# Kernel tuning notes

Hardware: AMD Instinct MI355X
Metric: run time of the kernel (lower is better)

Reference implementation:

```python
import jax, jax.numpy as jnp
import numpy as np

BN_EPS = 1e-5


def setup_inputs() -> dict:
    key = jax.random.key(0)
    ks = jax.random.split(key, 8)
    B, N, D = 16, 16384, 64
    NP, NS = 1024, 32
    inp = {
        "xyz": jax.random.normal(ks[0], (B, 3, N), dtype=jnp.float32),
        "points": jax.random.normal(ks[1], (B, D, N), dtype=jnp.float32),
        "fps_init": jax.random.randint(ks[2], (B,), 0, N, dtype=jnp.int32),
        "group_idx": jax.random.randint(ks[3], (B, NP, NS), 0, N, dtype=jnp.int32),
    }
    chans = [67, 64, 128, 128]
    for i in range(3):
        cin, cout = chans[i], chans[i + 1]
        wk = jax.random.fold_in(ks[4], i)
        inp[f"W{i}"] = jax.random.normal(wk, (cout, cin), dtype=jnp.float32) * (1.0 / np.sqrt(cin))
        inp[f"b{i}"] = jnp.zeros((cout,), dtype=jnp.float32)
        inp[f"g{i}"] = jnp.ones((cout,), dtype=jnp.float32)
        inp[f"be{i}"] = jnp.zeros((cout,), dtype=jnp.float32)
    return inp


def _fps(x, init_far, npoint):
    # x: [B,N,3]; iterative furthest point sampling, npoint sequential steps
    B, N, _ = x.shape

    def step(carry, _):
        dist, far = carry
        c = jnp.take_along_axis(x, far[:, None, None], axis=1)  # [B,1,3]
        d = jnp.sum((x - c) ** 2, axis=-1)                       # [B,N]
        dist = jnp.minimum(dist, d)
        return (dist, jnp.argmax(dist, axis=-1).astype(far.dtype)), far

    init = (jnp.full((B, N), 1e10, dtype=x.dtype), init_far)
    _, cents = jax.lax.scan(step, init, None, length=npoint)
    return cents.T  # [B, npoint]


def _conv_bn_relu(h, W, b, g, be):
    # h: [B, np, ns, Cin]; 1x1 conv == channel matmul; BN (training stats) over (B,np,ns)
    y = jnp.einsum('bskc,oc->bsko', h, W) + b
    m = y.mean(axis=(0, 1, 2))
    v = y.var(axis=(0, 1, 2))
    y = (y - m) * jax.lax.rsqrt(v + BN_EPS) * g + be
    return jax.nn.relu(y)


def reference(xyz, points, fps_init, group_idx,
              W0, b0, g0, be0, W1, b1, g1, be1, W2, b2, g2, be2):
    x = jnp.transpose(xyz, (0, 2, 1))     # [B,N,3]
    p = jnp.transpose(points, (0, 2, 1))  # [B,N,D]
    B, N, _ = x.shape
    NP, NS = group_idx.shape[1], group_idx.shape[2]

    cents = _fps(x, fps_init, NP)                                   # [B,NP]
    new_xyz = jnp.take_along_axis(x, cents[:, :, None], axis=1)     # [B,NP,3]

    flat = group_idx.reshape(B, NP * NS)
    gx = jnp.take_along_axis(x, flat[:, :, None], axis=1).reshape(B, NP, NS, 3)
    gp = jnp.take_along_axis(p, flat[:, :, None], axis=1).reshape(B, NP, NS, -1)
    h = jnp.concatenate([gx, gp], axis=-1)  # [B,NP,NS,67]

    h = _conv_bn_relu(h, W0, b0, g0, be0)
    h = _conv_bn_relu(h, W1, b1, g1, be1)
    h = _conv_bn_relu(h, W2, b2, g2, be2)
    new_points = h.max(axis=2)              # max over nsample -> [B,NP,Cout]

    return jnp.transpose(new_xyz, (0, 2, 1)), jnp.transpose(new_points, (0, 2, 1))
```

## Files before the change

kernel.cpp:

```cpp
#include <hip/hip_runtime.h>

typedef short bf16x8 __attribute__((ext_vector_type(8)));
typedef float f32x4 __attribute__((ext_vector_type(4)));
typedef float f32x2 __attribute__((ext_vector_type(2)));
typedef unsigned short u16;
typedef unsigned int u32;
typedef unsigned long long u64;

#define NPTS 16384
#define NPOINT 1024
#define STOT 524288
#define NCB 240
#define NW  960

__device__ __forceinline__ u16 f2bf(float f){
  u32 u = __builtin_bit_cast(u32, f);
  u += 0x7fffu + ((u >> 16) & 1u);
  return (u16)(u >> 16);
}
__device__ __forceinline__ float bf2f(u16 u){
  u32 x = ((u32)u) << 16;
  return __builtin_bit_cast(float, x);
}

template<int CTRL>
__device__ __forceinline__ float dpp_maxf(float v){
  int x = __builtin_amdgcn_update_dpp(0, __builtin_bit_cast(int, v), CTRL, 0xf, 0xf, true);
  return fmaxf(v, __builtin_bit_cast(float, x));
}
template<int CTRL>
__device__ __forceinline__ u64 dpp_max(u64 key){
  u32 lo = (u32)key, hi = (u32)(key >> 32);
  u32 lo1 = (u32)__builtin_amdgcn_update_dpp(0, (int)lo, CTRL, 0xf, 0xf, true);
  u32 hi1 = (u32)__builtin_amdgcn_update_dpp(0, (int)hi, CTRL, 0xf, 0xf, true);
  u64 k1 = ((u64)hi1 << 32) | (u64)lo1;
  return (k1 > key) ? k1 : key;
}
__device__ __forceinline__ u64 packkey(float d, int idx){
  return ((u64)__builtin_bit_cast(u32, d) << 32) | (u64)(u32)(~(u32)idx);
}

__device__ __forceinline__ void arrive(u32* c){
  __hip_atomic_fetch_add(c, 1u, __ATOMIC_RELEASE, __HIP_MEMORY_SCOPE_AGENT);
}
__device__ __forceinline__ void waitc(u32* c, u32 tgt){
  while (__hip_atomic_load(c, __ATOMIC_ACQUIRE, __HIP_MEMORY_SCOPE_AGENT) < tgt)
    __builtin_amdgcn_s_sleep(16);
}

struct FpsS  { uint2 wkey[2][16]; };
struct ConvS { float lsum[128]; float lsqr[128]; float av[128]; float dv[128]; };
union SMemU  { FpsS fps; ConvS conv; };

__device__ __forceinline__ bf16x8 load_bn_relu(const u16* __restrict__ row, int ko,
                                               const float* __restrict__ av,
                                               const float* __restrict__ dv){
  uint4 r = *(const uint4*)(row + ko);
  u32 w[4] = {r.x, r.y, r.z, r.w};
  bf16x8 out;
#pragma unroll
  for (int jj = 0; jj < 8; jj++){
    u16 us = (u16)(w[jj >> 1] >> ((jj & 1) * 16));
    float h = fmaxf(fmaf(av[ko + jj], bf2f(us), dv[ko + jj]), 0.f);
    out[jj] = (short)f2bf(h);
  }
  return out;
}

__global__ void zero_kernel(u32* __restrict__ ctrs){
  if (threadIdx.x < 64) ctrs[threadIdx.x] = 0;
}

__global__ __launch_bounds__(1024, 4) void mega_kernel(
    const float* __restrict__ xyz, const float* __restrict__ points,
    const int* __restrict__ finit, const int* __restrict__ gidx,
    const float* __restrict__ W0, const float* __restrict__ g0v, const float* __restrict__ be0,
    const float* __restrict__ W1, const float* __restrict__ g1v, const float* __restrict__ be1,
    const float* __restrict__ W2, const float* __restrict__ g2v, const float* __restrict__ be2,
    float* __restrict__ out0, float* __restrict__ out1,
    u16* __restrict__ XP, u16* __restrict__ y0, u16* __restrict__ y1,
    float* __restrict__ maxb, float* __restrict__ minb,
    float* __restrict__ statsF,
    u16* __restrict__ W0bf, u16* __restrict__ W1bf, u16* __restrict__ W2bf,
    u32* __restrict__ ctrs){
  __shared__ SMemU sm;
  const int t = threadIdx.x;
  const int wave = t >> 6, lane = t & 63;

  if (blockIdx.x < 16){
    const int b = blockIdx.x;
    const float* xb = xyz + (size_t)b * 3 * NPTS;
    f32x2 px[8], py[8], pz[8], dist[8];
#pragma unroll
    for (int j = 0; j < 8; j++){
      f32x2 x, y, z;
#pragma unroll
      for (int h = 0; h < 2; h++){
        int n = ((2*j + h) << 10) + t;
        x[h] = xb[n];
        y[h] = xb[NPTS + n];
        z[h] = xb[2*NPTS + n];
      }
      px[j] = x; py[j] = y; pz[j] = z;
      f32x2 big = {1e10f, 1e10f};
      dist[j] = big;
    }
    int nb = finit[b];
    float ccx = xb[nb], ccy = xb[NPTS + nb], ccz = xb[2*NPTS + nb];
    for (int it = 0; it < NPOINT; it++){
      const int p = it & 1;
      if (t == 0){
        out0[((size_t)b*3 + 0)*NPOINT + it] = ccx;
        out0[((size_t)b*3 + 1)*NPOINT + it] = ccy;
        out0[((size_t)b*3 + 2)*NPOINT + it] = ccz;
      }
      float bv = -1.f; int bk = 0;
      {
#pragma clang fp contract(off)
        f32x2 cx2 = {ccx, ccx}, cy2 = {ccy, ccy}, cz2 = {ccz, ccz};
#pragma unroll
        for (int j = 0; j < 8; j++){
          f32x2 dx = px[j] - cx2;
          f32x2 dy = py[j] - cy2;
          f32x2 dz = pz[j] - cz2;
          f32x2 dd = dx*dx + dy*dy + dz*dz;
          f32x2 dm = __builtin_elementwise_min(dist[j], dd);
          dist[j] = dm;
          bool g0 = dm.x > bv;
          bv = g0 ? dm.x : bv;  bk = g0 ? (2*j)   : bk;
          bool g1 = dm.y > bv;
          bv = g1 ? dm.y : bv;  bk = g1 ? (2*j+1) : bk;
        }
      }
      float m = bv;
      m = dpp_maxf<0xB1>(m);
      m = dpp_maxf<0x4E>(m);
      m = dpp_maxf<0x141>(m);
      m = dpp_maxf<0x140>(m);
      m = dpp_maxf<0x142>(m);
      m = dpp_maxf<0x143>(m);
      float ms = __builtin_bit_cast(float, __builtin_amdgcn_readlane(__builtin_bit_cast(int, m), 63));
      u64 mk = __ballot(bv == ms);
      u32 widx;
      if (__popcll(mk) == 1){
        int L = (int)__builtin_ctzll(mk);
        int kwin = __builtin_amdgcn_readlane(bk, L);
        widx = (u32)((kwin << 10) + (wave << 6) + L);
      } else {
        u64 key = packkey(bv, (bk << 10) + t);
        key = dpp_max<0xB1>(key); key = dpp_max<0x4E>(key);
        key = dpp_max<0x141>(key); key = dpp_max<0x140>(key);
        key = dpp_max<0x142>(key); key = dpp_max<0x143>(key);
        u32 lo = (u32)__builtin_amdgcn_readlane((int)(u32)key, 63);
        widx = ~lo;
      }
      if (lane == 0){
        uint2 wk; wk.x = widx; wk.y = __builtin_bit_cast(u32, ms);
        sm.fps.wkey[p][wave] = wk;
      }
      __syncthreads();
      uint2 wk = sm.fps.wkey[p][lane & 15];
      float wv = __builtin_bit_cast(float, wk.y);
      float g4 = wv;
      g4 = dpp_maxf<0xB1>(g4); g4 = dpp_maxf<0x4E>(g4);
      g4 = dpp_maxf<0x141>(g4); g4 = dpp_maxf<0x140>(g4);
      float gms = __builtin_bit_cast(float, __builtin_amdgcn_readfirstlane(__builtin_bit_cast(int, g4)));
      u64 mk2 = __ballot(wv == gms);
      u32 lo16 = (u32)mk2 & 0xFFFFu;
      if (__popc(lo16) == 1){
        int w = (int)__builtin_ctz(lo16);
        nb = __builtin_amdgcn_readlane((int)wk.x, w);
      } else {
        u64 k2 = ((u64)wk.y << 32) | (u64)(u32)(~wk.x);
        k2 = dpp_max<0xB1>(k2); k2 = dpp_max<0x4E>(k2);
        k2 = dpp_max<0x141>(k2); k2 = dpp_max<0x140>(k2);
        u32 lo = (u32)__builtin_amdgcn_readfirstlane((int)(u32)k2);
        nb = (int)~lo;
      }
      nb = __builtin_amdgcn_readfirstlane(nb);
      ccx = xb[nb]; ccy = xb[NPTS + nb]; ccz = xb[2*NPTS + nb];
    }
    return;
  }

  const int cb = blockIdx.x - 16;
  const int lw = wave & 3, g = wave >> 2;
  const int Wk = cb*4 + g;
  const int lrow = lane & 15, lq = lane >> 4;
  float* bsum0 = statsF;          float* bsqr0 = statsF + 8192;
  float* bsum1 = statsF + 16384;  float* bsqr1 = statsF + 24576;
  float* bsum2 = statsF + 32768;  float* bsqr2 = statsF + 40960;
  float* a0 = statsF + 49152;       float* d0 = a0 + 128;
  float* a1 = statsF + 49152 + 256; float* d1 = a1 + 128;
  float* a2 = statsF + 49152 + 512; float* d2 = a2 + 128;

  for (u32 idx = (u32)cb*1024u + t; idx < 16u*16384u; idx += (u32)NCB*1024u){
    u32 b = idx >> 14, n = idx & 16383u;
    const float* xb = xyz + (size_t)b*3*NPTS + n;
    const float* pb = points + (size_t)b*64*NPTS + n;
    u16* dst = XP + ((size_t)b*NPTS + n)*96;
#pragma unroll
    for (int half = 0; half < 2; half++){
      u32 w[24];
#pragma unroll
      for (int q = 0; q < 24; q++){
        int c0 = half*48 + 2*q, c1 = c0 + 1;
        float f0 = (c0 < 3) ? xb[(size_t)c0*NPTS] : (c0 < 67) ? pb[(size_t)(c0-3)*NPTS] : 0.f;
        float f1 = (c1 < 3) ? xb[(size_t)c1*NPTS] : (c1 < 67) ? pb[(size_t)(c1-3)*NPTS] : 0.f;
        w[q] = (u32)f2bf(f0) | ((u32)f2bf(f1) << 16);
      }
#pragma unroll
      for (int q = 0; q < 6; q++){
        uint4 v; v.x = w[4*q]; v.y = w[4*q+1]; v.z = w[4*q+2]; v.w = w[4*q+3];
        *(uint4*)(dst + half*48 + q*8) = v;
      }
    }
  }
  if (cb == 0){
    for (int i = t; i < 64*96; i += 1024){
      int nn = i / 96, kk = i % 96;
      W0bf[i] = (kk < 67) ? f2bf(W0[nn*67 + kk]) : (u16)0;
    }
    for (int i = t; i < 128*64; i += 1024) W1bf[i] = f2bf(W1[i]);
    for (int i = t; i < 128*128; i += 1024) W2bf[i] = f2bf(W2[i]);
  }
  if (cb == 1){
    for (int i = t; i < 49152; i += 1024) statsF[i] = 0.f;
  }
  __threadfence();
  __syncthreads();
  if (t == 0){ arrive(&ctrs[0]); waitc(&ctrs[0], NCB); }
  __syncthreads();

  if (t < 128){ sm.conv.lsum[t] = 0.f; sm.conv.lsqr[t] = 0.f; }
  __syncthreads();
  for (int j2 = Wk; j2 < 4096; j2 += NW){
    const int b = j2 >> 8;
    const size_t srow = (size_t)j2 * 128;
    const int gbase = b*32768 + (j2 & 255)*128;
    const int m0 = lw*32 + lrow, m1 = m0 + 16;
    const int p0 = gidx[gbase + m0];
    const int p1 = gidx[gbase + m1];
    const bf16x8* ar0 = (const bf16x8*)(XP + ((size_t)b*NPTS + p0)*96);
    const bf16x8* ar1 = (const bf16x8*)(XP + ((size_t)b*NPTS + p1)*96);
    f32x4 acc[2][4];
#pragma unroll
    for (int mt = 0; mt < 2; mt++)
#pragma unroll
      for (int nt = 0; nt < 4; nt++){ f32x4 z = {0.f,0.f,0.f,0.f}; acc[mt][nt] = z; }
#pragma unroll
    for (int ks = 0; ks < 3; ks++){
      bf16x8 af0 = ar0[ks*4 + lq];
      bf16x8 af1 = ar1[ks*4 + lq];
#pragma unroll
      for (int nt = 0; nt < 4; nt++){
        bf16x8 bb = *(const bf16x8*)(W0bf + (nt*16 + lrow)*96 + ks*32 + lq*8);
        acc[0][nt] = __builtin_amdgcn_mfma_f32_16x16x32_bf16(af0, bb, acc[0][nt], 0, 0, 0);
        acc[1][nt] = __builtin_amdgcn_mfma_f32_16x16x32_bf16(af1, bb, acc[1][nt], 0, 0, 0);
      }
    }
#pragma unroll
    for (int nt = 0; nt < 4; nt++){
      float s = 0.f, s2 = 0.f;
#pragma unroll
      for (int mt = 0; mt < 2; mt++){
#pragma unroll
        for (int i = 0; i < 4; i++){
          float u = acc[mt][nt][i];
          s += u; s2 = fmaf(u, u, s2);
          int m = lw*32 + mt*16 + lq*4 + i;
          y0[(srow + m)*64 + nt*16 + lrow] = f2bf(u);
        }
      }
      s  += __shfl_xor(s, 16, 64);  s  += __shfl_xor(s, 32, 64);
      s2 += __shfl_xor(s2, 16, 64); s2 += __shfl_xor(s2, 32, 64);
      if (lane < 16){ atomicAdd(&sm.conv.lsum[nt*16 + lane], s); atomicAdd(&sm.conv.lsqr[nt*16 + lane], s2); }
    }
  }
  __syncthreads();
  if (t < 64){
    atomicAdd(&bsum0[(cb & 63)*128 + t], sm.conv.lsum[t]);
    atomicAdd(&bsqr0[(cb & 63)*128 + t], sm.conv.lsqr[t]);
  }
  __threadfence();
  __syncthreads();
  if (t == 0) arrive(&ctrs[1]);
  if (cb == 0){
    if (t == 0) waitc(&ctrs[1], NCB);
    __syncthreads();
    if (t < 64){
      float s = 0.f, s2 = 0.f;
      for (int k = 0; k < 64; k++){ s += bsum0[k*128 + t]; s2 += bsqr0[k*128 + t]; }
      const float inv = 1.f / (float)STOT;
      float m = s * inv, v = s2 * inv - m*m;
      float aa = g0v[t] / sqrtf(v + 1e-5f);
      a0[t] = aa; d0[t] = be0[t] - m*aa;
    }
    __threadfence();
    __syncthreads();
    if (t == 0) arrive(&ctrs[2]);
  }
  if (t == 0) waitc(&ctrs[2], 1);
  __syncthreads();

  if (t < 128){ sm.conv.lsum[t] = 0.f; sm.conv.lsqr[t] = 0.f; }
  if (t < 64){ sm.conv.av[t] = a0[t]; sm.conv.dv[t] = d0[t]; }
  __syncthreads();
  for (int j2 = Wk; j2 < 4096; j2 += NW){
    const size_t srow = (size_t)j2 * 128;
    const int m0 = lw*32 + lrow, m1 = m0 + 16;
    const u16* row0 = y0 + (srow + m0)*64;
    const u16* row1 = y0 + (srow + m1)*64;
    f32x4 acc[2][8];
#pragma unroll
    for (int mt = 0; mt < 2; mt++)
#pragma unroll
      for (int nt = 0; nt < 8; nt++){ f32x4 z = {0.f,0.f,0.f,0.f}; acc[mt][nt] = z; }
#pragma unroll
    for (int ks = 0; ks < 2; ks++){
      const int ko = ks*32 + lq*8;
      bf16x8 af0 = load_bn_relu(row0, ko, sm.conv.av, sm.conv.dv);
      bf16x8 af1 = load_bn_relu(row1, ko, sm.conv.av, sm.conv.dv);
#pragma unroll
      for (int nt = 0; nt < 8; nt++){
        bf16x8 bb = *(const bf16x8*)(W1bf + (nt*16 + lrow)*64 + ko);
        acc[0][nt] = __builtin_amdgcn_mfma_f32_16x16x32_bf16(af0, bb, acc[0][nt], 0, 0, 0);
        acc[1][nt] = __builtin_amdgcn_mfma_f32_16x16x32_bf16(af1, bb, acc[1][nt], 0, 0, 0);
      }
    }
#pragma unroll
    for (int nt = 0; nt < 8; nt++){
      float s = 0.f, s2 = 0.f;
#pragma unroll
      for (int mt = 0; mt < 2; mt++){
#pragma unroll
        for (int i = 0; i < 4; i++){
          float u = acc[mt][nt][i];
          s += u; s2 = fmaf(u, u, s2);
          int m = lw*32 + mt*16 + lq*4 + i;
          y1[(srow + m)*128 + nt*16 + lrow] = f2bf(u);
        }
      }
      s  += __shfl_xor(s, 16, 64);  s  += __shfl_xor(s, 32, 64);
      s2 += __shfl_xor(s2, 16, 64); s2 += __shfl_xor(s2, 32, 64);
      if (lane < 16){ atomicAdd(&sm.conv.lsum[nt*16 + lane], s); atomicAdd(&sm.conv.lsqr[nt*16 + lane], s2); }
    }
  }
  __syncthreads();
  if (t < 128){
    atomicAdd(&bsum1[(cb & 63)*128 + t], sm.conv.lsum[t]);
    atomicAdd(&bsqr1[(cb & 63)*128 + t], sm.conv.lsqr[t]);
  }
  __threadfence();
  __syncthreads();
  if (t == 0) arrive(&ctrs[3]);
  if (cb == 0){
    if (t == 0) waitc(&ctrs[3], NCB);
    __syncthreads();
    if (t < 128){
      float s = 0.f, s2 = 0.f;
      for (int k = 0; k < 64; k++){ s += bsum1[k*128 + t]; s2 += bsqr1[k*128 + t]; }
      const float inv = 1.f / (float)STOT;
      float m = s * inv, v = s2 * inv - m*m;
      float aa = g1v[t] / sqrtf(v + 1e-5f);
      a1[t] = aa; d1[t] = be1[t] - m*aa;
    }
    __threadfence();
    __syncthreads();
    if (t == 0) arrive(&ctrs[4]);
  }
  if (t == 0) waitc(&ctrs[4], 1);
  __syncthreads();

  if (t < 128){ sm.conv.lsum[t] = 0.f; sm.conv.lsqr[t] = 0.f;
                sm.conv.av[t] = a1[t]; sm.conv.dv[t] = d1[t]; }
  __syncthreads();
  for (int j2 = Wk; j2 < 4096; j2 += NW){
    const size_t srow = (size_t)j2 * 128;
    const int m0 = lw*32 + lrow, m1 = m0 + 16;
    const u16* row0 = y1 + (srow + m0)*128;
    const u16* row1 = y1 + (srow + m1)*128;
    f32x4 acc[2][8];
#pragma unroll
    for (int mt = 0; mt < 2; mt++)
#pragma unroll
      for (int nt = 0; nt < 8; nt++){ f32x4 z = {0.f,0.f,0.f,0.f}; acc[mt][nt] = z; }
#pragma unroll
    for (int ks = 0; ks < 4; ks++){
      const int ko = ks*32 + lq*8;
      bf16x8 af0 = load_bn_relu(row0, ko, sm.conv.av, sm.conv.dv);
      bf16x8 af1 = load_bn_relu(row1, ko, sm.conv.av, sm.conv.dv);
#pragma unroll
      for (int nt = 0; nt < 8; nt++){
        bf16x8 bb = *(const bf16x8*)(W2bf + (nt*16 + lrow)*128 + ko);
        acc[0][nt] = __builtin_amdgcn_mfma_f32_16x16x32_bf16(af0, bb, acc[0][nt], 0, 0, 0);
        acc[1][nt] = __builtin_amdgcn_mfma_f32_16x16x32_bf16(af1, bb, acc[1][nt], 0, 0, 0);
      }
    }
#pragma unroll
    for (int nt = 0; nt < 8; nt++){
      float s = 0.f, s2 = 0.f, mx = -3.4e38f, mn = 3.4e38f;
#pragma unroll
      for (int mt = 0; mt < 2; mt++){
#pragma unroll
        for (int i = 0; i < 4; i++){
          float u = acc[mt][nt][i];
          s += u; s2 = fmaf(u, u, s2);
          mx = fmaxf(mx, u); mn = fminf(mn, u);
        }
      }
      s  += __shfl_xor(s, 16, 64);  s  += __shfl_xor(s, 32, 64);
      s2 += __shfl_xor(s2, 16, 64); s2 += __shfl_xor(s2, 32, 64);
      mx = fmaxf(mx, __shfl_xor(mx, 16, 64)); mx = fmaxf(mx, __shfl_xor(mx, 32, 64));
      mn = fminf(mn, __shfl_xor(mn, 16, 64)); mn = fminf(mn, __shfl_xor(mn, 32, 64));
      if (lane < 16){
        size_t gi = ((size_t)j2*4 + lw)*128 + nt*16 + lane;
        maxb[gi] = mx; minb[gi] = mn;
        atomicAdd(&sm.conv.lsum[nt*16 + lane], s); atomicAdd(&sm.conv.lsqr[nt*16 + lane], s2);
      }
    }
  }
  __syncthreads();
  if (t < 128){
    atomicAdd(&bsum2[(cb & 63)*128 + t], sm.conv.lsum[t]);
    atomicAdd(&bsqr2[(cb & 63)*128 + t], sm.conv.lsqr[t]);
  }
  __threadfence();
  __syncthreads();
  if (t == 0) arrive(&ctrs[5]);
  if (cb == 0){
    if (t == 0) waitc(&ctrs[5], NCB);
    __syncthreads();
    if (t < 128){
      float s = 0.f, s2 = 0.f;
      for (int k = 0; k < 64; k++){ s += bsum2[k*128 + t]; s2 += bsqr2[k*128 + t]; }
      const float inv = 1.f / (float)STOT;
      float m = s * inv, v = s2 * inv - m*m;
      float aa = g2v[t] / sqrtf(v + 1e-5f);
      a2[t] = aa; d2[t] = be2[t] - m*aa;
    }
    __threadfence();
    __syncthreads();
    if (t == 0) arrive(&ctrs[6]);
  }
  if (t == 0) waitc(&ctrs[6], 1);
  __syncthreads();

  for (u32 e = (u32)cb*1024u + t; e < 16u*1024u*128u; e += (u32)NCB*1024u){
    u32 np = e & 1023u;
    u32 c  = (e >> 10) & 127u;
    u32 b  = e >> 17;
    size_t gi = ((size_t)b*1024 + np)*128 + c;
    float a = a2[c];
    float v = (a >= 0.f) ? maxb[gi] : minb[gi];
    out1[((size_t)b*128 + c)*1024 + np] = fmaxf(fmaf(a, v, d2[c]), 0.f);
  }
}

extern "C" void kernel_launch(void* const* d_in, const int* in_sizes, int n_in,
                              void* d_out, int out_size, void* d_ws, size_t ws_size,
                              hipStream_t stream) {
  const float* xyz    = (const float*)d_in[0];
  const float* points = (const float*)d_in[1];
  const int*   finit  = (const int*)d_in[2];
  const int*   gidx   = (const int*)d_in[3];
  const float* W0  = (const float*)d_in[4];
  const float* g0v = (const float*)d_in[6];
  const float* be0 = (const float*)d_in[7];
  const float* W1  = (const float*)d_in[8];
  const float* g1v = (const float*)d_in[10];
  const float* be1 = (const float*)d_in[11];
  const float* W2  = (const float*)d_in[12];
  const float* g2v = (const float*)d_in[14];
  const float* be2 = (const float*)d_in[15];

  float* out0 = (float*)d_out;
  float* out1 = out0 + 16*3*NPOINT;

  char* ws = (char*)d_ws;
  u16* y1 = (u16*)ws;
  u16* XP = (u16*)ws;
  u16* y0 = (u16*)(ws + 134217728);
  float* maxb = (float*)(ws + 134217728);
  float* minb = (float*)(ws + 134217728 + 8388608);
  float* statsF = (float*)(ws + 201326592);
  u16* W0bf = (u16*)(ws + 201326592 + 49920*4);
  u16* W1bf = W0bf + 64*96;
  u16* W2bf = W1bf + 128*64;
  u32* ctrs = (u32*)(ws + 205782016);

  zero_kernel<<<1, 64, 0, stream>>>(ctrs);
  mega_kernel<<<256, 1024, 0, stream>>>(
      xyz, points, finit, gidx,
      W0, g0v, be0, W1, g1v, be1, W2, g2v, be2,
      out0, out1, XP, y0, y1, maxb, minb, statsF,
      W0bf, W1bf, W2bf, ctrs);
}
```

Baseline: 2.379 ms.

## Pass FPS winner coordinates through LDS instead of reloading from global

In the furthest point sampling loop, the winning lane of each wave now writes its 24 register-held coordinates and its packed key into shared memory. After the barrier every thread reduces the 16 wave keys and reads the new centroid's coordinates straight from shared memory, which removes a dependent global load from the serial per-iteration critical path. Centroid outputs are buffered in LDS and written out once after the loop rather than stored to global every iteration. This enlarges the shared-memory footprint (about 20 KB) and adds per-iteration LDS writes from one lane per wave.

```diff
diff --git a/kernel.cpp b/kernel.cpp
--- a/kernel.cpp
+++ b/kernel.cpp
@@ -48,7 +48,7 @@
     __builtin_amdgcn_s_sleep(16);
 }
 
-struct FpsS  { uint2 wkey[2][16]; };
+struct FpsS  { u32 rec[2][16][64]; float cbuf[NPOINT][3]; };
 struct ConvS { float lsum[128]; float lsqr[128]; float av[128]; float dv[128]; };
 union SMemU  { FpsS fps; ConvS conv; };
 
@@ -105,14 +105,15 @@
       f32x2 big = {1e10f, 1e10f};
       dist[j] = big;
     }
-    int nb = finit[b];
-    float ccx = xb[nb], ccy = xb[NPTS + nb], ccz = xb[2*NPTS + nb];
+    const int far0 = finit[b];
+    float ccx = xb[far0], ccy = xb[NPTS + far0], ccz = xb[2*NPTS + far0];
+
     for (int it = 0; it < NPOINT; it++){
       const int p = it & 1;
       if (t == 0){
-        out0[((size_t)b*3 + 0)*NPOINT + it] = ccx;
-        out0[((size_t)b*3 + 1)*NPOINT + it] = ccy;
-        out0[((size_t)b*3 + 2)*NPOINT + it] = ccz;
+        sm.fps.cbuf[it][0] = ccx;
+        sm.fps.cbuf[it][1] = ccy;
+        sm.fps.cbuf[it][2] = ccz;
       }
       float bv = -1.f; int bk = 0;
       {
@@ -141,44 +142,42 @@
       m = dpp_maxf<0x143>(m);
       float ms = __builtin_bit_cast(float, __builtin_amdgcn_readlane(__builtin_bit_cast(int, m), 63));
       u64 mk = __ballot(bv == ms);
-      u32 widx;
+      int wl;
       if (__popcll(mk) == 1){
-        int L = (int)__builtin_ctzll(mk);
-        int kwin = __builtin_amdgcn_readlane(bk, L);
-        widx = (u32)((kwin << 10) + (wave << 6) + L);
+        wl = (int)__builtin_ctzll(mk);
       } else {
         u64 key = packkey(bv, (bk << 10) + t);
         key = dpp_max<0xB1>(key); key = dpp_max<0x4E>(key);
         key = dpp_max<0x141>(key); key = dpp_max<0x140>(key);
         key = dpp_max<0x142>(key); key = dpp_max<0x143>(key);
         u32 lo = (u32)__builtin_amdgcn_readlane((int)(u32)key, 63);
-        widx = ~lo;
-      }
-      if (lane == 0){
-        uint2 wk; wk.x = widx; wk.y = __builtin_bit_cast(u32, ms);
-        sm.fps.wkey[p][wave] = wk;
+        wl = (int)((~lo) & 63u);
+      }
+      if (lane == wl){
+        u32* r = &sm.fps.rec[p][wave][0];
+#pragma unroll
+        for (int j = 0; j < 8; j++){
+          *(f32x2*)(r + 2*j)      = px[j];
+          *(f32x2*)(r + 16 + 2*j) = py[j];
+          *(f32x2*)(r + 32 + 2*j) = pz[j];
+        }
+        *(u64*)(r + 48) = packkey(bv, (bk << 10) + t);
       }
       __syncthreads();
-      uint2 wk = sm.fps.wkey[p][lane & 15];
-      float wv = __builtin_bit_cast(float, wk.y);
-      float g4 = wv;
-      g4 = dpp_maxf<0xB1>(g4); g4 = dpp_maxf<0x4E>(g4);
-      g4 = dpp_maxf<0x141>(g4); g4 = dpp_maxf<0x140>(g4);
-      float gms = __builtin_bit_cast(float, __builtin_amdgcn_readfirstlane(__builtin_bit_cast(int, g4)));
-      u64 mk2 = __ballot(wv == gms);
-      u32 lo16 = (u32)mk2 & 0xFFFFu;
-      if (__popc(lo16) == 1){
-        int w = (int)__builtin_ctz(lo16);
-        nb = __builtin_amdgcn_readlane((int)wk.x, w);
-      } else {
-        u64 k2 = ((u64)wk.y << 32) | (u64)(u32)(~wk.x);
-        k2 = dpp_max<0xB1>(k2); k2 = dpp_max<0x4E>(k2);
-        k2 = dpp_max<0x141>(k2); k2 = dpp_max<0x140>(k2);
-        u32 lo = (u32)__builtin_amdgcn_readfirstlane((int)(u32)k2);
-        nb = (int)~lo;
-      }
-      nb = __builtin_amdgcn_readfirstlane(nb);
-      ccx = xb[nb]; ccy = xb[NPTS + nb]; ccz = xb[2*NPTS + nb];
+      u64 gk = *(const u64*)(&sm.fps.rec[p][lane & 15][48]);
+      gk = dpp_max<0xB1>(gk); gk = dpp_max<0x4E>(gk);
+      gk = dpp_max<0x141>(gk); gk = dpp_max<0x140>(gk);
+      u32 n = ~(u32)gk;
+      int w    = (int)((n >> 6) & 15u);
+      int kwin = (int)(n >> 10);
+      const u32* rr = &sm.fps.rec[p][w][0];
+      ccx = *(const float*)(rr + kwin);
+      ccy = *(const float*)(rr + 16 + kwin);
+      ccz = *(const float*)(rr + 32 + kwin);
+    }
+    for (int i = t; i < 3 * NPOINT; i += 1024){
+      int cc = i >> 10, itt = i & 1023;
+      out0[((size_t)b*3 + cc)*NPOINT + itt] = sm.fps.cbuf[itt][cc];
     }
     return;
   }
```

Result: faster. 2.202 ms (-7.5%).

## Spatially sort FPS points per wave and prune waves via bounding-box distance

Applied to the files above, without the earlier changes.

Before the FPS loop, the points are bucketed into a coarse Morton-like spatial order using a shared-memory histogram and counting sort. Each wave then holds a spatially compact cluster, sorted by index, and keeps its bounding box. On each iteration a wave skips the distance update when the new centroid's box distance cannot lower its current max min-distance, and reuses its cached winner key. The winning point's coordinates are broadcast from registers through LDS instead of reloaded from global memory, and centroid outputs are buffered in LDS and written once at the end. This costs an extra __syncthreads per iteration and setup sorting work, and tie-breaking now depends on the original index carried through the sort.

```diff
diff --git a/kernel.cpp b/kernel.cpp
--- a/kernel.cpp
+++ b/kernel.cpp
@@ -2,7 +2,6 @@
 
 typedef short bf16x8 __attribute__((ext_vector_type(8)));
 typedef float f32x4 __attribute__((ext_vector_type(4)));
-typedef float f32x2 __attribute__((ext_vector_type(2)));
 typedef unsigned short u16;
 typedef unsigned int u32;
 typedef unsigned long long u64;
@@ -27,6 +26,21 @@
 __device__ __forceinline__ float dpp_maxf(float v){
   int x = __builtin_amdgcn_update_dpp(0, __builtin_bit_cast(int, v), CTRL, 0xf, 0xf, true);
   return fmaxf(v, __builtin_bit_cast(float, x));
+}
+template<int CTRL>
+__device__ __forceinline__ float dpp_minf(float v){
+  int x = __builtin_amdgcn_update_dpp(0, __builtin_bit_cast(int, v), CTRL, 0xf, 0xf, true);
+  return fminf(v, __builtin_bit_cast(float, x));
+}
+__device__ __forceinline__ float wave_maxf(float v){
+  v = dpp_maxf<0xB1>(v); v = dpp_maxf<0x4E>(v); v = dpp_maxf<0x141>(v);
+  v = dpp_maxf<0x140>(v); v = dpp_maxf<0x142>(v); v = dpp_maxf<0x143>(v);
+  return __builtin_bit_cast(float, __builtin_amdgcn_readlane(__builtin_bit_cast(int, v), 63));
+}
+__device__ __forceinline__ float wave_minf(float v){
+  v = dpp_minf<0xB1>(v); v = dpp_minf<0x4E>(v); v = dpp_minf<0x141>(v);
+  v = dpp_minf<0x140>(v); v = dpp_minf<0x142>(v); v = dpp_minf<0x143>(v);
+  return __builtin_bit_cast(float, __builtin_amdgcn_readlane(__builtin_bit_cast(int, v), 63));
 }
 template<int CTRL>
 __device__ __forceinline__ u64 dpp_max(u64 key){
@@ -36,9 +50,6 @@
   u64 k1 = ((u64)hi1 << 32) | (u64)lo1;
   return (k1 > key) ? k1 : key;
 }
-__device__ __forceinline__ u64 packkey(float d, int idx){
-  return ((u64)__builtin_bit_cast(u32, d) << 32) | (u64)(u32)(~(u32)idx);
-}
 
 __device__ __forceinline__ void arrive(u32* c){
   __hip_atomic_fetch_add(c, 1u, __ATOMIC_RELEASE, __HIP_MEMORY_SCOPE_AGENT);
@@ -48,7 +59,18 @@
     __builtin_amdgcn_s_sleep(16);
 }
 
-struct FpsS  { uint2 wkey[2][16]; };
+struct FpsRun {
+  float cbuf[NPOINT][3];
+  uint2 wkey[2][16];
+  u32   wroute[2][16];
+  float4 csl[2];
+};
+struct FpsSrt {
+  u32 hist[256];
+  float red[16][6];
+  u32 sidx[16384];
+};
+struct FpsS  { union { FpsRun run; FpsSrt srt; } u; };
 struct ConvS { float lsum[128]; float lsqr[128]; float av[128]; float dv[128]; };
 union SMemU  { FpsS fps; ConvS conv; };
 
@@ -90,76 +112,191 @@
   if (blockIdx.x < 16){
     const int b = blockIdx.x;
     const float* xb = xyz + (size_t)b * 3 * NPTS;
-    f32x2 px[8], py[8], pz[8], dist[8];
-#pragma unroll
-    for (int j = 0; j < 8; j++){
-      f32x2 x, y, z;
-#pragma unroll
-      for (int h = 0; h < 2; h++){
-        int n = ((2*j + h) << 10) + t;
-        x[h] = xb[n];
-        y[h] = xb[NPTS + n];
-        z[h] = xb[2*NPTS + n];
-      }
-      px[j] = x; py[j] = y; pz[j] = z;
-      f32x2 big = {1e10f, 1e10f};
-      dist[j] = big;
-    }
-    int nb = finit[b];
-    float ccx = xb[nb], ccy = xb[NPTS + nb], ccz = xb[2*NPTS + nb];
+    float px[16], py[16], pz[16], dist[16];
+    u32 opk[8];
+
+    float mnx = 1e30f, mxx = -1e30f, mny = 1e30f, mxy = -1e30f, mnz = 1e30f, mxz = -1e30f;
+#pragma unroll
+    for (int k = 0; k < 16; k++){
+      int n = (k << 10) + t;
+      float x = xb[n], y = xb[NPTS + n], z = xb[2*NPTS + n];
+      px[k] = x; py[k] = y; pz[k] = z;
+      mnx = fminf(mnx, x); mxx = fmaxf(mxx, x);
+      mny = fminf(mny, y); mxy = fmaxf(mxy, y);
+      mnz = fminf(mnz, z); mxz = fmaxf(mxz, z);
+    }
+    mnx = wave_minf(mnx); mxx = wave_maxf(mxx);
+    mny = wave_minf(mny); mxy = wave_maxf(mxy);
+    mnz = wave_minf(mnz); mxz = wave_maxf(mxz);
+    if (lane == 0){
+      sm.fps.u.srt.red[wave][0] = mnx; sm.fps.u.srt.red[wave][1] = mxx;
+      sm.fps.u.srt.red[wave][2] = mny; sm.fps.u.srt.red[wave][3] = mxy;
+      sm.fps.u.srt.red[wave][4] = mnz; sm.fps.u.srt.red[wave][5] = mxz;
+    }
+    for (int i = t; i < 256; i += 1024) sm.fps.u.srt.hist[i] = 0;
+    __syncthreads();
+#pragma unroll
+    for (int w = 0; w < 16; w++){
+      mnx = fminf(mnx, sm.fps.u.srt.red[w][0]); mxx = fmaxf(mxx, sm.fps.u.srt.red[w][1]);
+      mny = fminf(mny, sm.fps.u.srt.red[w][2]); mxy = fmaxf(mxy, sm.fps.u.srt.red[w][3]);
+      mnz = fminf(mnz, sm.fps.u.srt.red[w][4]); mxz = fmaxf(mxz, sm.fps.u.srt.red[w][5]);
+    }
+    const float sclx = 7.9999f / fmaxf(mxx - mnx, 1e-20f);
+    const float scly = 7.9999f / fmaxf(mxy - mny, 1e-20f);
+    const float sclz = 3.9999f / fmaxf(mxz - mnz, 1e-20f);
+
+    u32 kq[16];
+#pragma unroll
+    for (int k = 0; k < 16; k++){
+      int xq = (int)((px[k] - mnx) * sclx); xq = min(max(xq, 0), 7);
+      int yq = (int)((py[k] - mny) * scly); yq = min(max(yq, 0), 7);
+      int zq = (int)((pz[k] - mnz) * sclz); zq = min(max(zq, 0), 3);
+      u32 key = ((u32)(xq >> 2) << 7) | ((u32)(yq >> 2) << 6) |
+                ((u32)((xq >> 1) & 1) << 5) | ((u32)((yq >> 1) & 1) << 4) |
+                ((u32)((zq >> 1) & 1) << 3) |
+                ((u32)(xq & 1) << 2) | ((u32)(yq & 1) << 1) | (u32)(zq & 1);
+      kq[k] = key;
+      atomicAdd(&sm.fps.u.srt.hist[key], 1u);
+    }
+    __syncthreads();
+    if (t == 0){
+      u32 run2 = 0;
+      for (int i = 0; i < 256; i++){ u32 c = sm.fps.u.srt.hist[i]; sm.fps.u.srt.hist[i] = run2; run2 += c; }
+    }
+    __syncthreads();
+#pragma unroll
+    for (int k = 0; k < 16; k++){
+      u32 pos = atomicAdd(&sm.fps.u.srt.hist[kq[k]], 1u);
+      sm.fps.u.srt.sidx[pos] = (u32)((k << 10) + t);
+    }
+    __syncthreads();
+    u32 o[16];
+#pragma unroll
+    for (int k = 0; k < 16; k++)
+      o[k] = sm.fps.u.srt.sidx[(wave << 10) + (k << 6) + lane] & 16383u;
+    __syncthreads();
+#pragma unroll
+    for (int P = 1; P < 16; P <<= 1){
+#pragma unroll
+      for (int K = P; K >= 1; K >>= 1){
+#pragma unroll
+        for (int J = K & (P - 1); J + K < 16; J += 2*K){
+#pragma unroll
+          for (int I = 0; I < K; I++){
+            if ((I + J + K < 16) && ((I + J) / (2*P) == (I + J + K) / (2*P))){
+              u32 a = o[I + J], c2 = o[I + J + K];
+              o[I + J] = min(a, c2); o[I + J + K] = max(a, c2);
+            }
+          }
+        }
+      }
+    }
+#pragma unroll
+    for (int j = 0; j < 8; j++) opk[j] = o[2*j] | (o[2*j + 1] << 16);
+    float wlx = 1e30f, whx = -1e30f, wly = 1e30f, why = -1e30f, wlz = 1e30f, whz = -1e30f;
+#pragma unroll
+    for (int k = 0; k < 16; k++){
+      float x = xb[o[k]], y = xb[NPTS + o[k]], z = xb[2*NPTS + o[k]];
+      px[k] = x; py[k] = y; pz[k] = z; dist[k] = 1e10f;
+      wlx = fminf(wlx, x); whx = fmaxf(whx, x);
+      wly = fminf(wly, y); why = fmaxf(why, y);
+      wlz = fminf(wlz, z); whz = fmaxf(whz, z);
+    }
+    const float lox = wave_minf(wlx), hix = wave_maxf(whx);
+    const float loy = wave_minf(wly), hiy = wave_maxf(why);
+    const float loz = wave_minf(wlz), hiz = wave_maxf(whz);
+    const int far0 = finit[b];
+    if (t == 0){
+      sm.fps.u.run.csl[0] = make_float4(xb[far0], xb[NPTS + far0], xb[2*NPTS + far0], 0.f);
+    }
+    float bvw = 1e10f;
+    uint2 cck = make_uint2(0u, 0u); u32 ccrt = 0u;
+    __syncthreads();
+
     for (int it = 0; it < NPOINT; it++){
       const int p = it & 1;
+      float4 cc = sm.fps.u.run.csl[p];
       if (t == 0){
-        out0[((size_t)b*3 + 0)*NPOINT + it] = ccx;
-        out0[((size_t)b*3 + 1)*NPOINT + it] = ccy;
-        out0[((size_t)b*3 + 2)*NPOINT + it] = ccz;
-      }
-      float bv = -1.f; int bk = 0;
-      {
+        sm.fps.u.run.cbuf[it][0] = cc.x;
+        sm.fps.u.run.cbuf[it][1] = cc.y;
+        sm.fps.u.run.cbuf[it][2] = cc.z;
+      }
+      float dlx = fmaxf(fmaxf(lox - cc.x, cc.x - hix), 0.f);
+      float dly = fmaxf(fmaxf(loy - cc.y, cc.y - hiy), 0.f);
+      float dlz = fmaxf(fmaxf(loz - cc.z, cc.z - hiz), 0.f);
+      float d2 = dlx*dlx + dly*dly + dlz*dlz;
+      bool prune = (d2 * 0.99999f >= bvw);
+      uint2 outkey; u32 outrt;
+      if (!prune){
+        float bv = -1.f; int bk = 0;
+        {
 #pragma clang fp contract(off)
-        f32x2 cx2 = {ccx, ccx}, cy2 = {ccy, ccy}, cz2 = {ccz, ccz};
-#pragma unroll
-        for (int j = 0; j < 8; j++){
-          f32x2 dx = px[j] - cx2;
-          f32x2 dy = py[j] - cy2;
-          f32x2 dz = pz[j] - cz2;
-          f32x2 dd = dx*dx + dy*dy + dz*dz;
-          f32x2 dm = __builtin_elementwise_min(dist[j], dd);
-          dist[j] = dm;
-          bool g0 = dm.x > bv;
-          bv = g0 ? dm.x : bv;  bk = g0 ? (2*j)   : bk;
-          bool g1 = dm.y > bv;
-          bv = g1 ? dm.y : bv;  bk = g1 ? (2*j+1) : bk;
+#pragma unroll
+          for (int k = 0; k < 16; k++){
+            float dx = px[k] - cc.x;
+            float dy = py[k] - cc.y;
+            float dz = pz[k] - cc.z;
+            float dd = dx*dx + dy*dy + dz*dz;
+            float dm = fminf(dist[k], dd);
+            dist[k] = dm;
+            bool g = dm > bv;
+            bv = g ? dm : bv;  bk = g ? k : bk;
+          }
         }
-      }
-      float m = bv;
-      m = dpp_maxf<0xB1>(m);
-      m = dpp_maxf<0x4E>(m);
-      m = dpp_maxf<0x141>(m);
-      m = dpp_maxf<0x140>(m);
-      m = dpp_maxf<0x142>(m);
-      m = dpp_maxf<0x143>(m);
-      float ms = __builtin_bit_cast(float, __builtin_amdgcn_readlane(__builtin_bit_cast(int, m), 63));
-      u64 mk = __ballot(bv == ms);
-      u32 widx;
-      if (__popcll(mk) == 1){
-        int L = (int)__builtin_ctzll(mk);
-        int kwin = __builtin_amdgcn_readlane(bk, L);
-        widx = (u32)((kwin << 10) + (wave << 6) + L);
+        float ms = wave_maxf(bv);
+        u64 mk = __ballot(bv == ms);
+        int L, kwin; u32 oidx;
+        if (__popcll(mk) == 1){
+          L = (int)__builtin_ctzll(mk);
+          kwin = __builtin_amdgcn_readlane(bk, L);
+          u32 s0 = (u32)__builtin_amdgcn_readlane((int)opk[0], L);
+          u32 s1 = (u32)__builtin_amdgcn_readlane((int)opk[1], L);
+          u32 s2 = (u32)__builtin_amdgcn_readlane((int)opk[2], L);
+          u32 s3 = (u32)__builtin_amdgcn_readlane((int)opk[3], L);
+          u32 s4 = (u32)__builtin_amdgcn_readlane((int)opk[4], L);
+          u32 s5 = (u32)__builtin_amdgcn_readlane((int)opk[5], L);
+          u32 s6 = (u32)__builtin_amdgcn_readlane((int)opk[6], L);
+          u32 s7 = (u32)__builtin_amdgcn_readlane((int)opk[7], L);
+          int kh = kwin >> 1;
+          u32 osel = s0;
+          osel = (kh == 1) ? s1 : osel; osel = (kh == 2) ? s2 : osel;
+          osel = (kh == 3) ? s3 : osel; osel = (kh == 4) ? s4 : osel;
+          osel = (kh == 5) ? s5 : osel; osel = (kh == 6) ? s6 : osel;
+          osel = (kh == 7) ? s7 : osel;
+          oidx = (osel >> ((kwin & 1) << 4)) & 0xFFFFu;
+        } else {
+          int bh = bk >> 1;
+          u32 po = opk[0];
+          po = (bh == 1) ? opk[1] : po; po = (bh == 2) ? opk[2] : po;
+          po = (bh == 3) ? opk[3] : po; po = (bh == 4) ? opk[4] : po;
+          po = (bh == 5) ? opk[5] : po; po = (bh == 6) ? opk[6] : po;
+          po = (bh == 7) ? opk[7] : po;
+          u32 myo = (po >> ((bk & 1) << 4)) & 0xFFFFu;
+          u64 mykey = ((u64)__builtin_bit_cast(u32, bv) << 32) | (u64)(~myo);
+          u64 kr = mykey;
+          kr = dpp_max<0xB1>(kr); kr = dpp_max<0x4E>(kr);
+          kr = dpp_max<0x141>(kr); kr = dpp_max<0x140>(kr);
+          kr = dpp_max<0x142>(kr); kr = dpp_max<0x143>(kr);
+          u32 wlo = (u32)__builtin_amdgcn_readlane((int)(u32)kr, 63);
+          u32 whi = (u32)__builtin_amdgcn_readlane((int)(u32)(kr >> 32), 63);
+          u64 win = ((u64)whi << 32) | (u64)wlo;
+          L = (int)__builtin_ctzll(__ballot(mykey == win));
+          kwin = __builtin_amdgcn_readlane(bk, L);
+          oidx = (~wlo) & 0xFFFFu;
+        }
+        outkey.x = ~oidx; outkey.y = __builtin_bit_cast(u32, ms);
+        outrt = ((u32)L << 4) | (u32)kwin;
+        bvw = ms; cck = outkey; ccrt = outrt;
       } else {
-        u64 key = packkey(bv, (bk << 10) + t);
-        key = dpp_max<0xB1>(key); key = dpp_max<0x4E>(key);
-        key = dpp_max<0x141>(key); key = dpp_max<0x140>(key);
-        key = dpp_max<0x142>(key); key = dpp_max<0x143>(key);
-        u32 lo = (u32)__builtin_amdgcn_readlane((int)(u32)key, 63);
-        widx = ~lo;
+        outkey = cck; outrt = ccrt;
       }
       if (lane == 0){
-        uint2 wk; wk.x = widx; wk.y = __builtin_bit_cast(u32, ms);
-        sm.fps.wkey[p][wave] = wk;
+        sm.fps.u.run.wkey[p][wave] = outkey;
+        sm.fps.u.run.wroute[p][wave] = outrt;
       }
       __syncthreads();
-      uint2 wk = sm.fps.wkey[p][lane & 15];
+      uint2 wk = sm.fps.u.run.wkey[p][lane & 15];
+      u32 rta = sm.fps.u.run.wroute[p][lane & 15];
       float wv = __builtin_bit_cast(float, wk.y);
       float g4 = wv;
       g4 = dpp_maxf<0xB1>(g4); g4 = dpp_maxf<0x4E>(g4);
@@ -167,18 +304,35 @@
       float gms = __builtin_bit_cast(float, __builtin_amdgcn_readfirstlane(__builtin_bit_cast(int, g4)));
       u64 mk2 = __ballot(wv == gms);
       u32 lo16 = (u32)mk2 & 0xFFFFu;
+      int wstar;
       if (__popc(lo16) == 1){
-        int w = (int)__builtin_ctz(lo16);
-        nb = __builtin_amdgcn_readlane((int)wk.x, w);
+        wstar = (int)__builtin_ctz(lo16);
       } else {
-        u64 k2 = ((u64)wk.y << 32) | (u64)(u32)(~wk.x);
-        k2 = dpp_max<0xB1>(k2); k2 = dpp_max<0x4E>(k2);
-        k2 = dpp_max<0x141>(k2); k2 = dpp_max<0x140>(k2);
-        u32 lo = (u32)__builtin_amdgcn_readfirstlane((int)(u32)k2);
-        nb = (int)~lo;
-      }
-      nb = __builtin_amdgcn_readfirstlane(nb);
-      ccx = xb[nb]; ccy = xb[NPTS + nb]; ccz = xb[2*NPTS + nb];
+        u64 mykey2 = ((u64)wk.y << 32) | (u64)wk.x;
+        u64 kr = mykey2;
+        kr = dpp_max<0xB1>(kr); kr = dpp_max<0x4E>(kr);
+        kr = dpp_max<0x141>(kr); kr = dpp_max<0x140>(kr);
+        u32 wlo = (u32)__builtin_amdgcn_readfirstlane((int)(u32)kr);
+        u32 whi = (u32)__builtin_amdgcn_readfirstlane((int)(u32)(kr >> 32));
+        u64 win = ((u64)whi << 32) | (u64)wlo;
+        wstar = (int)__builtin_ctz((u32)__ballot(mykey2 == win) & 0xFFFFu);
+      }
+      u32 rt = (u32)__builtin_amdgcn_readlane((int)rta, wstar);
+      if (wave == wstar && lane == (int)(rt >> 4)){
+        int kk = (int)(rt & 15u);
+        float sx = px[0], sy = py[0], sz = pz[0];
+#pragma unroll
+        for (int k = 1; k < 16; k++){
+          bool e = (kk == k);
+          sx = e ? px[k] : sx; sy = e ? py[k] : sy; sz = e ? pz[k] : sz;
+        }
+        sm.fps.u.run.csl[p ^ 1] = make_float4(sx, sy, sz, 0.f);
+      }
+      __syncthreads();
+    }
+    for (int i = t; i < 3 * NPOINT; i += 1024){
+      int cc2 = i >> 10, itt = i & 1023;
+      out0[((size_t)b*3 + cc2)*NPOINT + itt] = sm.fps.u.run.cbuf[itt][cc2];
     }
     return;
   }
```

New measurement: 2.047 ms. 1.16x faster.
